# Kernel tuning notes

Measured on AMD Instinct MI355X. Metric: run time of the kernel, lower is better.

## Reference

```python
import jax, jax.numpy as jnp
import numpy as np

N_NODES = 500_000
N_EDGES = 16_000_000
F_IN, F_HID, F_OUT = 5, 5, 8


def _gcn_conv(x, W, b, src, dst, norm, n):
    # x: [N, Fin] -> transform first (cheaper than transforming messages)
    h = x @ W                              # [N, Fout]
    msg = h[src] * norm[:, None]           # [E', Fout] gather + per-edge scale
    out = jax.ops.segment_sum(msg, dst, num_segments=n)  # scatter-add over dst
    return out + b


def setup_inputs() -> dict:
    key = jax.random.key(0)
    ks = jax.random.split(key, 6)
    x = jax.random.normal(ks[0], (N_NODES, F_IN), dtype=jnp.float32)
    edge_index = jax.random.randint(ks[1], (2, N_EDGES), 0, N_NODES, dtype=jnp.int32)
    # Glorot-ish init for the two GCNConv layers
    W1 = jax.random.normal(ks[2], (F_IN, F_HID), dtype=jnp.float32) / np.sqrt(F_IN)
    b1 = jnp.zeros((F_HID,), dtype=jnp.float32)
    W2 = jax.random.normal(ks[3], (F_HID, F_OUT), dtype=jnp.float32) / np.sqrt(F_HID)
    b2 = jnp.zeros((F_OUT,), dtype=jnp.float32)
    return {"x": x, "edge_index": edge_index, "W1": W1, "b1": b1, "W2": W2, "b2": b2}


def reference(x, edge_index, W1, b1, W2, b2):
    n = x.shape[0]
    # GCNConv default: add self-loops, symmetric D^-1/2 A D^-1/2 normalization
    loops = jnp.arange(n, dtype=edge_index.dtype)
    src = jnp.concatenate([edge_index[0], loops])
    dst = jnp.concatenate([edge_index[1], loops])
    deg = jax.ops.segment_sum(jnp.ones_like(dst, dtype=x.dtype), dst, num_segments=n)
    dinv = jnp.where(deg > 0, jax.lax.rsqrt(deg), 0.0)
    norm = dinv[src] * dinv[dst]           # [E + N]

    h = _gcn_conv(x, W1, b1, src, dst, norm, n)
    h = jax.nn.relu(h)
    # F.dropout with training=False is the identity (eval-mode reference)
    h = _gcn_conv(h, W2, b2, src, dst, norm, n)
    return jax.nn.log_softmax(h, axis=1)
```

## Files before the change

### kernel.cpp

```cpp
#include <hip/hip_runtime.h>
#include <math.h>


#define FIN 5
#define FHID 5
#define FOUT 8
#define RB 256
#define EPA 24576
#define NBUCK_MAX 2048
#define OCAP 10240

typedef _Float16 half8 __attribute__((ext_vector_type(8)));
typedef int int4v __attribute__((ext_vector_type(4)));
typedef float fl4 __attribute__((ext_vector_type(4)));


__global__ void k_scan1(const int* __restrict__ t, int* __restrict__ scn,
                        int* __restrict__ partial, int n) {
    __shared__ int sh[256];
    int tx = threadIdx.x;
    int i = blockIdx.x * 256 + tx;
    int v = (i < n) ? t[i] : 0;
    sh[tx] = v;
    __syncthreads();
    for (int off = 1; off < 256; off <<= 1) {
        int add = (tx >= off) ? sh[tx - off] : 0;
        __syncthreads();
        sh[tx] += add;
        __syncthreads();
    }
    if (i < n) scn[i] = sh[tx] - v;
    if (tx == 255) partial[blockIdx.x] = sh[255];
}

__global__ void k_scan2(int* __restrict__ partial, int nb) {
    __shared__ int sh[256];
    __shared__ int carry;
    int tx = threadIdx.x;
    if (tx == 0) carry = 0;
    __syncthreads();
    for (int base = 0; base < nb; base += 256) {
        int i = base + tx;
        int v = (i < nb) ? partial[i] : 0;
        int c0 = carry;
        sh[tx] = v;
        __syncthreads();
        for (int off = 1; off < 256; off <<= 1) {
            int add = (tx >= off) ? sh[tx - off] : 0;
            __syncthreads();
            sh[tx] += add;
            __syncthreads();
        }
        if (i < nb) partial[i] = c0 + sh[tx] - v;
        __syncthreads();
        if (tx == 0) carry = c0 + sh[255];
        __syncthreads();
    }
}


__global__ void k_histA(const int* __restrict__ dst, int* __restrict__ cnt,
                        int e, int nbuck, int nblkA) {
    __shared__ int hist[NBUCK_MAX];
    int tx = threadIdx.x, blk = blockIdx.x;
    for (int b = tx; b < nbuck; b += 1024) hist[b] = 0;
    __syncthreads();
    size_t base = (size_t)blk * EPA;
    const int4v* dst4 = (const int4v*)dst;
    for (int k = 0; k < EPA / 4096; ++k) {
        size_t e4 = base / 4 + (size_t)k * 1024 + tx;
        size_t i = e4 * 4;
        if (i + 3 < (size_t)e) {
            int4v d4 = __builtin_nontemporal_load(&dst4[e4]);
#pragma unroll
            for (int j = 0; j < 4; ++j) atomicAdd(&hist[d4[j] >> 8], 1);
        } else {
            for (int j = 0; j < 4; ++j) {
                size_t ii = i + j;
                if (ii < (size_t)e) atomicAdd(&hist[dst[ii] >> 8], 1);
            }
        }
    }
    __syncthreads();
    for (int b = tx; b < nbuck; b += 1024) cnt[(size_t)b * nblkA + blk] = hist[b];
}

__global__ void k_scatterA(const int* __restrict__ src, const int* __restrict__ dst,
                           const int* __restrict__ cnt,
                           const int* __restrict__ scn, const int* __restrict__ part,
                           unsigned int* __restrict__ binnedA,
                           int e, int nbuck, int nblkA) {
    __shared__ int lstart[NBUCK_MAX];
    __shared__ int cur[NBUCK_MAX];
    __shared__ int gbase[NBUCK_MAX];
    __shared__ unsigned int staged[EPA];
    int tx = threadIdx.x, blk = blockIdx.x;
    for (int b = tx; b < NBUCK_MAX; b += 1024) {
        if (b < nbuck) {
            size_t idx = (size_t)b * nblkA + blk;
            lstart[b] = cnt[idx];
            gbase[b] = scn[idx] + part[idx >> 8];
        } else {
            lstart[b] = 0;
        }
    }
    __syncthreads();
    int j0 = tx, j1 = tx + 1024;
    int c0 = lstart[j0], c1 = lstart[j1];
    for (int off = 1; off < NBUCK_MAX; off <<= 1) {
        int a0 = (j0 >= off) ? lstart[j0 - off] : 0;
        int a1 = (j1 >= off) ? lstart[j1 - off] : 0;
        __syncthreads();
        lstart[j0] += a0; lstart[j1] += a1;
        __syncthreads();
    }
    int e0 = lstart[j0] - c0, e1 = lstart[j1] - c1;
    __syncthreads();
    lstart[j0] = e0; lstart[j1] = e1;
    cur[j0] = e0;    cur[j1] = e1;
    __syncthreads();
    size_t base = (size_t)blk * EPA;
    const int4v* dst4 = (const int4v*)dst;
    const int4v* src4 = (const int4v*)src;
    for (int k = 0; k < EPA / 4096; ++k) {
        size_t e4 = base / 4 + (size_t)k * 1024 + tx;
        size_t i = e4 * 4;
        if (i + 3 < (size_t)e) {
            int4v d4 = __builtin_nontemporal_load(&dst4[e4]);
            int4v s4 = __builtin_nontemporal_load(&src4[e4]);
#pragma unroll
            for (int j = 0; j < 4; ++j) {
                int d = d4[j];
                int pos = atomicAdd(&cur[d >> 8], 1);
                staged[pos] = ((unsigned int)(d & (RB - 1)) << 19) | (unsigned int)s4[j];
            }
        } else {
            for (int j = 0; j < 4; ++j) {
                size_t ii = i + j;
                if (ii < (size_t)e) {
                    int d = dst[ii];
                    int pos = atomicAdd(&cur[d >> 8], 1);
                    staged[pos] = ((unsigned int)(d & (RB - 1)) << 19) | (unsigned int)src[ii];
                }
            }
        }
    }
    __syncthreads();
    int grp = tx >> 4, lane = tx & 15;
    for (int b = grp; b < nbuck; b += 64) {
        int ls = lstart[b];
        int le = (b + 1 < NBUCK_MAX) ? lstart[b + 1] : 0;
        int len = le - ls;
        int gb = gbase[b];
        for (int k = lane; k < len; k += 16)
            binnedA[gb + k] = staged[ls + k];
    }
}


__global__ void k_passC(const unsigned int* __restrict__ binnedA,
                        const int* __restrict__ scn, const int* __restrict__ part,
                        const float* __restrict__ x,
                        half8* __restrict__ g1, unsigned int* __restrict__ binned3,
                        int* __restrict__ nodeptr, int* __restrict__ midptr,
                        int n, int e, int nbuck, int nblkA, unsigned int half) {
    __shared__ int hist[2 * RB];
    __shared__ int scanbuf[2 * RB];
    __shared__ int cur[2 * RB];
    __shared__ unsigned int obuf[OCAP];
    int tx = threadIdx.x, b = blockIdx.x;
    hist[tx] = 0;
    __syncthreads();
    size_t i0 = (size_t)b * nblkA;
    int start = scn[i0] + part[i0 >> 8];
    int end;
    if (b + 1 < nbuck) {
        size_t i1 = (size_t)(b + 1) * nblkA;
        end = scn[i1] + part[i1 >> 8];
    } else {
        end = e;
    }
    int len = end - start;
    for (int i = start + tx; i < end; i += 512) {
        unsigned int p = binnedA[i];
        int key = (int)((p >> 19) << 1) | ((p & 0x7FFFFu) >= half ? 1 : 0);
        atomicAdd(&hist[key], 1);
    }
    __syncthreads();
    int v = hist[tx];
    scanbuf[tx] = v;
    __syncthreads();
    for (int off = 1; off < 2 * RB; off <<= 1) {
        int add = (tx >= off) ? scanbuf[tx - off] : 0;
        __syncthreads();
        scanbuf[tx] += add;
        __syncthreads();
    }
    int excl = scanbuf[tx] - v;
    cur[tx] = excl;
    if ((tx & 1) == 0) nodeptr[(size_t)b * RB + (tx >> 1)] = start + excl;
    else               midptr[(size_t)b * RB + (tx >> 1)]  = start + excl;
    if (tx < RB) {
        int node = b * RB + tx;
        if (node < n) {
            int deg = hist[2 * tx] + hist[2 * tx + 1];
            float d = rsqrtf((float)(deg + 1));
            const float* xp = x + (size_t)node * FIN;
            half8 row = {};
#pragma unroll
            for (int f = 0; f < FIN; ++f) row[f] = (_Float16)(xp[f] * d);
            row[5] = (_Float16)d;
            g1[node] = row;
        }
    }
    if (b == nbuck - 1 && tx == 0) nodeptr[(size_t)nbuck * RB] = end;
    __syncthreads();
    if (len <= OCAP) {
        for (int i = start + tx; i < end; i += 512) {
            unsigned int p = binnedA[i];
            int key = (int)((p >> 19) << 1) | ((p & 0x7FFFFu) >= half ? 1 : 0);
            int pos = atomicAdd(&cur[key], 1);
            obuf[pos] = p & 0x7FFFFu;
        }
        __syncthreads();
        for (int j = tx; j < len; j += 512)
            binned3[start + j] = obuf[j];
    } else {
        for (int i = start + tx; i < end; i += 512) {
            unsigned int p = binnedA[i];
            int key = (int)((p >> 19) << 1) | ((p & 0x7FFFFu) >= half ? 1 : 0);
            int pos = atomicAdd(&cur[key], 1);
            binned3[start + pos] = p & 0x7FFFFu;
        }
    }
}


__global__ void k_vphase0(const unsigned int* __restrict__ ed,
                          const int* __restrict__ nodeptr, const int* __restrict__ midptr,
                          const half8* __restrict__ g,
                          fl4* __restrict__ acc4, float* __restrict__ acc1, int n) {
    int tid = blockIdx.x * blockDim.x + threadIdx.x;
    int node = tid >> 4;
    int lane = tid & 15;
    if (node >= n) return;
    int o0 = nodeptr[node];
    int om = midptr[node];
    float a0 = 0, a1 = 0, a2 = 0, a3 = 0, a4 = 0;
    for (int k = o0 + lane; k < om; k += 16) {
        unsigned int s = __builtin_nontemporal_load(&ed[k]);
        half8 hv = g[s];
        a0 += (float)hv[0]; a1 += (float)hv[1]; a2 += (float)hv[2];
        a3 += (float)hv[3]; a4 += (float)hv[4];
    }
#pragma unroll
    for (int off = 1; off < 16; off <<= 1) {
        a0 += __shfl_xor(a0, off, 16);
        a1 += __shfl_xor(a1, off, 16);
        a2 += __shfl_xor(a2, off, 16);
        a3 += __shfl_xor(a3, off, 16);
        a4 += __shfl_xor(a4, off, 16);
    }
    if (lane == 0) {
        fl4 p; p.x = a0; p.y = a1; p.z = a2; p.w = a3;
        __builtin_nontemporal_store(p, &acc4[node]);
        __builtin_nontemporal_store(a4, &acc1[node]);
    }
}

__global__ void k_vp1_l1(const unsigned int* __restrict__ ed,
                         const int* __restrict__ nodeptr, const int* __restrict__ midptr,
                         const half8* __restrict__ g1,
                         const fl4* __restrict__ acc4, const float* __restrict__ acc1,
                         const float* __restrict__ W1, const float* __restrict__ b1,
                         half8* __restrict__ g2, int n) {
    int tid = blockIdx.x * blockDim.x + threadIdx.x;
    int node = tid >> 4;
    int lane = tid & 15;
    if (node >= n) return;
    int om = midptr[node];
    int o1 = nodeptr[node + 1];
    float a0 = 0, a1 = 0, a2 = 0, a3 = 0, a4 = 0;
    for (int k = om + lane; k < o1; k += 16) {
        unsigned int s = __builtin_nontemporal_load(&ed[k]);
        half8 hv = g1[s];
        a0 += (float)hv[0]; a1 += (float)hv[1]; a2 += (float)hv[2];
        a3 += (float)hv[3]; a4 += (float)hv[4];
    }
#pragma unroll
    for (int off = 1; off < 16; off <<= 1) {
        a0 += __shfl_xor(a0, off, 16);
        a1 += __shfl_xor(a1, off, 16);
        a2 += __shfl_xor(a2, off, 16);
        a3 += __shfl_xor(a3, off, 16);
        a4 += __shfl_xor(a4, off, 16);
    }
    if (lane == 0) {
        fl4 pp = acc4[node];
        float p4 = acc1[node];
        half8 gi = g1[node];
        float d = (float)gi[5];
        float v[FIN];
        v[0] = (a0 + pp.x + (float)gi[0]) * d;
        v[1] = (a1 + pp.y + (float)gi[1]) * d;
        v[2] = (a2 + pp.z + (float)gi[2]) * d;
        v[3] = (a3 + pp.w + (float)gi[3]) * d;
        v[4] = (a4 + p4   + (float)gi[4]) * d;
        half8 go = {};
#pragma unroll
        for (int j = 0; j < FHID; ++j) {
            float s = b1[j];
#pragma unroll
            for (int k = 0; k < FIN; ++k) s = fmaf(v[k], W1[k * FHID + j], s);
            go[j] = (_Float16)(fmaxf(s, 0.0f) * d);
        }
        go[5] = gi[5];
        g2[node] = go;
    }
}

__global__ void k_vp1_l2(const unsigned int* __restrict__ ed,
                         const int* __restrict__ nodeptr, const int* __restrict__ midptr,
                         const half8* __restrict__ g2,
                         const fl4* __restrict__ acc4, const float* __restrict__ acc1,
                         const float* __restrict__ W2, const float* __restrict__ b2,
                         float* __restrict__ out, int n) {
    int tid = blockIdx.x * blockDim.x + threadIdx.x;
    int node = tid >> 4;
    int lane = tid & 15;
    if (node >= n) return;
    int om = midptr[node];
    int o1 = nodeptr[node + 1];
    float a0 = 0, a1 = 0, a2 = 0, a3 = 0, a4 = 0;
    for (int k = om + lane; k < o1; k += 16) {
        unsigned int s = __builtin_nontemporal_load(&ed[k]);
        half8 hv = g2[s];
        a0 += (float)hv[0]; a1 += (float)hv[1]; a2 += (float)hv[2];
        a3 += (float)hv[3]; a4 += (float)hv[4];
    }
#pragma unroll
    for (int off = 1; off < 16; off <<= 1) {
        a0 += __shfl_xor(a0, off, 16);
        a1 += __shfl_xor(a1, off, 16);
        a2 += __shfl_xor(a2, off, 16);
        a3 += __shfl_xor(a3, off, 16);
        a4 += __shfl_xor(a4, off, 16);
    }
    if (lane == 0) {
        fl4 pp = acc4[node];
        float p4 = acc1[node];
        half8 gi = g2[node];
        float d = (float)gi[5];
        float v[FHID];
        v[0] = (a0 + pp.x + (float)gi[0]) * d;
        v[1] = (a1 + pp.y + (float)gi[1]) * d;
        v[2] = (a2 + pp.z + (float)gi[2]) * d;
        v[3] = (a3 + pp.w + (float)gi[3]) * d;
        v[4] = (a4 + p4   + (float)gi[4]) * d;
        float o[FOUT];
        float m = -1e30f;
#pragma unroll
        for (int j = 0; j < FOUT; ++j) {
            float s = b2[j];
#pragma unroll
            for (int k = 0; k < FHID; ++k) s = fmaf(v[k], W2[k * FOUT + j], s);
            o[j] = s;
            m = fmaxf(m, s);
        }
        float ssum = 0.0f;
#pragma unroll
        for (int j = 0; j < FOUT; ++j) ssum += expf(o[j] - m);
        float lse = m + logf(ssum);
        float* op = out + (size_t)node * FOUT;
#pragma unroll
        for (int j = 0; j < FOUT; ++j) op[j] = o[j] - lse;
    }
}


__global__ void f_init_deg(float* __restrict__ deg, int n) {
    int i = blockIdx.x * blockDim.x + threadIdx.x;
    if (i < n) deg[i] = 1.0f;
}
__global__ void f_count_deg(const int* __restrict__ dst, float* __restrict__ deg, int e) {
    int i = blockIdx.x * blockDim.x + threadIdx.x;
    if (i < e) atomicAdd(&deg[dst[i]], 1.0f);
}
__global__ void f_finish_deg_g1(const float* __restrict__ x, float* __restrict__ dinv,
                                float* __restrict__ g1, int n) {
    int i = blockIdx.x * blockDim.x + threadIdx.x;
    if (i >= n) return;
    float d = rsqrtf(dinv[i]);
    dinv[i] = d;
#pragma unroll
    for (int f = 0; f < FIN; ++f) g1[(size_t)i * FIN + f] = x[(size_t)i * FIN + f] * d;
}
__global__ void f_scatter5(const int* __restrict__ src, const int* __restrict__ dst,
                           const float* __restrict__ g, float* __restrict__ acc, int e) {
    int i = blockIdx.x * blockDim.x + threadIdx.x;
    if (i >= e) return;
    int s = src[i], d = dst[i];
    float* a = acc + (size_t)d * 5;
    const float* gp = g + (size_t)s * 5;
    atomicAdd(a + 0, gp[0]);
    atomicAdd(a + 1, gp[1]);
    atomicAdd(a + 2, gp[2]);
    atomicAdd(a + 3, gp[3]);
    atomicAdd(a + 4, gp[4]);
}
__global__ void f_update1(const float* __restrict__ dinv, float* __restrict__ g,
                          float* __restrict__ acc, const float* __restrict__ W1,
                          const float* __restrict__ b1, int n) {
    int i = blockIdx.x * blockDim.x + threadIdx.x;
    if (i >= n) return;
    float d = dinv[i];
    float v[FIN];
#pragma unroll
    for (int f = 0; f < FIN; ++f) {
        size_t idx = (size_t)i * FIN + f;
        v[f] = (acc[idx] + g[idx]) * d;
        acc[idx] = 0.0f;
    }
#pragma unroll
    for (int j = 0; j < FHID; ++j) {
        float s = b1[j];
#pragma unroll
        for (int k = 0; k < FIN; ++k) s += v[k] * W1[k * FHID + j];
        g[(size_t)i * FHID + j] = fmaxf(s, 0.0f) * d;
    }
}
__global__ void f_update2(const float* __restrict__ dinv, const float* __restrict__ g,
                          const float* __restrict__ acc, const float* __restrict__ W2,
                          const float* __restrict__ b2, float* __restrict__ out, int n) {
    int i = blockIdx.x * blockDim.x + threadIdx.x;
    if (i >= n) return;
    float d = dinv[i];
    float v[FHID];
#pragma unroll
    for (int f = 0; f < FHID; ++f) v[f] = (acc[(size_t)i * FHID + f] + g[(size_t)i * FHID + f]) * d;
    float o[FOUT];
    float m = -1e30f;
#pragma unroll
    for (int j = 0; j < FOUT; ++j) {
        float s = b2[j];
#pragma unroll
        for (int k = 0; k < FHID; ++k) s += v[k] * W2[k * FOUT + j];
        o[j] = s;
        m = fmaxf(m, s);
    }
    float ssum = 0.0f;
#pragma unroll
    for (int j = 0; j < FOUT; ++j) ssum += expf(o[j] - m);
    float lse = m + logf(ssum);
#pragma unroll
    for (int j = 0; j < FOUT; ++j) out[(size_t)i * FOUT + j] = o[j] - lse;
}


extern "C" void kernel_launch(void* const* d_in, const int* in_sizes, int n_in,
                              void* d_out, int out_size, void* d_ws, size_t ws_size,
                              hipStream_t stream) {
    const float* x  = (const float*)d_in[0];
    const int*   ei = (const int*)d_in[1];
    const float* W1 = (const float*)d_in[2];
    const float* b1 = (const float*)d_in[3];
    const float* W2 = (const float*)d_in[4];
    const float* b2 = (const float*)d_in[5];

    const int n = in_sizes[0] / FIN;
    const int e = in_sizes[1] / 2;
    const int* src = ei;
    const int* dst = ei + e;

    const int nbuck = (n + RB - 1) / RB;
    const int nblkA = (e + EPA - 1) / EPA;
    const size_t m = (size_t)nbuck * nblkA;
    const int nsb = (int)((m + 255) / 256);

    size_t off = 0;
    auto al = [&](size_t bytes) { size_t o = off; off = (off + bytes + 15) & ~(size_t)15; return o; };
    int*          cnt     = (int*)((char*)d_ws + al(m * 4));
    int*          scn     = (int*)((char*)d_ws + al(m * 4));
    int*          part    = (int*)((char*)d_ws + al((size_t)nsb * 4));
    int*          nptr    = (int*)((char*)d_ws + al(((size_t)nbuck * RB + 1) * 4));
    int*          mptr    = (int*)((char*)d_ws + al((size_t)nbuck * RB * 4));
    half8*        g1      = (half8*)((char*)d_ws + al((size_t)n * 16));
    unsigned int* binnedA = (unsigned int*)((char*)d_ws + al((size_t)e * 4));
    unsigned int* binned3 = (unsigned int*)((char*)d_ws + al((size_t)e * 4));
    half8*        g2      = (half8*)binnedA;
    fl4*          acc4    = (fl4*)((char*)binnedA + (size_t)16 * 1024 * 1024);
    float*        acc1    = (float*)((char*)binnedA + (size_t)32 * 1024 * 1024);
    const size_t need = off;

    if (ws_size >= need && n <= 524288 && n >= 1 && (e & 3) == 0 && nbuck <= NBUCK_MAX &&
        (size_t)e * 4 >= (size_t)34 * 1024 * 1024 && (size_t)n * 16 <= (size_t)16 * 1024 * 1024) {
        const unsigned int half = (unsigned int)(n >> 1);
        k_histA<<<nblkA, 1024, 0, stream>>>(dst, cnt, e, nbuck, nblkA);
        k_scan1<<<nsb, 256, 0, stream>>>(cnt, scn, part, (int)m);
        k_scan2<<<1, 256, 0, stream>>>(part, nsb);
        k_scatterA<<<nblkA, 1024, 0, stream>>>(src, dst, cnt, scn, part, binnedA, e, nbuck, nblkA);
        k_passC<<<nbuck, 512, 0, stream>>>(binnedA, scn, part, x, g1, binned3, nptr, mptr,
                                           n, e, nbuck, nblkA, half);
        const int ga = (int)(((size_t)n * 16 + 511) / 512);
        k_vphase0<<<ga, 512, 0, stream>>>(binned3, nptr, mptr, g1, acc4, acc1, n);
        k_vp1_l1<<<ga, 512, 0, stream>>>(binned3, nptr, mptr, g1, acc4, acc1, W1, b1, g2, n);
        k_vphase0<<<ga, 512, 0, stream>>>(binned3, nptr, mptr, g2, acc4, acc1, n);
        k_vp1_l2<<<ga, 512, 0, stream>>>(binned3, nptr, mptr, g2, acc4, acc1, W2, b2, (float*)d_out, n);
        return;
    }

    const int B = 256;
    const int gn = (n + B - 1) / B;
    const int ge = (e + B - 1) / B;
    float* fdinv = (float*)d_ws;
    float* fg    = fdinv + n;
    float* facc  = fg + (size_t)5 * n;
    hipMemsetAsync(facc, 0, (size_t)5 * n * sizeof(float), stream);
    f_init_deg<<<gn, B, 0, stream>>>(fdinv, n);
    f_count_deg<<<ge, B, 0, stream>>>(dst, fdinv, e);
    f_finish_deg_g1<<<gn, B, 0, stream>>>(x, fdinv, fg, n);
    f_scatter5<<<ge, B, 0, stream>>>(src, dst, fg, facc, e);
    f_update1<<<gn, B, 0, stream>>>(fdinv, fg, facc, W1, b1, n);
    f_scatter5<<<ge, B, 0, stream>>>(src, dst, fg, facc, e);
    f_update2<<<gn, B, 0, stream>>>(fdinv, fg, facc, W2, b2, (float*)d_out, n);
}
```

Baseline: 489.8 us.

## Halve per-node lanes, scan counts in place, shrink scatter tile, parallelize softmax

The gather kernels now use 8 lanes per node instead of 16. The average degree is about 32, so this gives fewer idle lanes and half the thread count. The final layer spreads the 8 output logits and the log-softmax across the 8 lanes instead of running them serially in lane 0. The bucket-count scan now runs in place, and scatterA derives local counts from adjacent scanned offsets, which drops one workspace array and one read. EPA is halved, which doubles the number of scatter blocks and cuts shared staging per block; in exchange the count matrix and the scan work get larger.

```diff
diff --git a/kernel.cpp b/kernel.cpp
--- a/kernel.cpp
+++ b/kernel.cpp
@@ -6,7 +6,7 @@
 #define FHID 5
 #define FOUT 8
 #define RB 256
-#define EPA 24576
+#define EPA 12288
 #define NBUCK_MAX 2048
 #define OCAP 10240
 
@@ -15,12 +15,11 @@
 typedef float fl4 __attribute__((ext_vector_type(4)));
 
 
-__global__ void k_scan1(const int* __restrict__ t, int* __restrict__ scn,
-                        int* __restrict__ partial, int n) {
+__global__ void k_scan1(int* __restrict__ data, int* __restrict__ partial, int n) {
     __shared__ int sh[256];
     int tx = threadIdx.x;
     int i = blockIdx.x * 256 + tx;
-    int v = (i < n) ? t[i] : 0;
+    int v = (i < n) ? data[i] : 0;
     sh[tx] = v;
     __syncthreads();
     for (int off = 1; off < 256; off <<= 1) {
@@ -29,7 +28,7 @@
         sh[tx] += add;
         __syncthreads();
     }
-    if (i < n) scn[i] = sh[tx] - v;
+    if (i < n) data[i] = sh[tx] - v;
     if (tx == 255) partial[blockIdx.x] = sh[255];
 }
 
@@ -86,7 +85,6 @@
 }
 
 __global__ void k_scatterA(const int* __restrict__ src, const int* __restrict__ dst,
-                           const int* __restrict__ cnt,
                            const int* __restrict__ scn, const int* __restrict__ part,
                            unsigned int* __restrict__ binnedA,
                            int e, int nbuck, int nblkA) {
@@ -95,11 +93,15 @@
     __shared__ int gbase[NBUCK_MAX];
     __shared__ unsigned int staged[EPA];
     int tx = threadIdx.x, blk = blockIdx.x;
+    const size_t mm = (size_t)nbuck * nblkA;
     for (int b = tx; b < NBUCK_MAX; b += 1024) {
         if (b < nbuck) {
             size_t idx = (size_t)b * nblkA + blk;
-            lstart[b] = cnt[idx];
-            gbase[b] = scn[idx] + part[idx >> 8];
+            int s0 = scn[idx] + part[idx >> 8];
+            size_t idx1 = idx + 1;
+            int s1 = (idx1 < mm) ? (scn[idx1] + part[idx1 >> 8]) : e;
+            gbase[b] = s0;
+            lstart[b] = s1 - s0;
         } else {
             lstart[b] = 0;
         }
@@ -146,13 +148,13 @@
         }
     }
     __syncthreads();
-    int grp = tx >> 4, lane = tx & 15;
-    for (int b = grp; b < nbuck; b += 64) {
+    int grp = tx >> 3, lane = tx & 7;
+    for (int b = grp; b < nbuck; b += 128) {
         int ls = lstart[b];
         int le = (b + 1 < NBUCK_MAX) ? lstart[b + 1] : 0;
         int len = le - ls;
         int gb = gbase[b];
-        for (int k = lane; k < len; k += 16)
+        for (int k = lane; k < len; k += 8)
             binnedA[gb + k] = staged[ls + k];
     }
 }
@@ -241,25 +243,25 @@
                           const half8* __restrict__ g,
                           fl4* __restrict__ acc4, float* __restrict__ acc1, int n) {
     int tid = blockIdx.x * blockDim.x + threadIdx.x;
-    int node = tid >> 4;
-    int lane = tid & 15;
+    int node = tid >> 3;
+    int lane = tid & 7;
     if (node >= n) return;
     int o0 = nodeptr[node];
     int om = midptr[node];
     float a0 = 0, a1 = 0, a2 = 0, a3 = 0, a4 = 0;
-    for (int k = o0 + lane; k < om; k += 16) {
+    for (int k = o0 + lane; k < om; k += 8) {
         unsigned int s = __builtin_nontemporal_load(&ed[k]);
         half8 hv = g[s];
         a0 += (float)hv[0]; a1 += (float)hv[1]; a2 += (float)hv[2];
         a3 += (float)hv[3]; a4 += (float)hv[4];
     }
 #pragma unroll
-    for (int off = 1; off < 16; off <<= 1) {
-        a0 += __shfl_xor(a0, off, 16);
-        a1 += __shfl_xor(a1, off, 16);
-        a2 += __shfl_xor(a2, off, 16);
-        a3 += __shfl_xor(a3, off, 16);
-        a4 += __shfl_xor(a4, off, 16);
+    for (int off = 1; off < 8; off <<= 1) {
+        a0 += __shfl_xor(a0, off, 8);
+        a1 += __shfl_xor(a1, off, 8);
+        a2 += __shfl_xor(a2, off, 8);
+        a3 += __shfl_xor(a3, off, 8);
+        a4 += __shfl_xor(a4, off, 8);
     }
     if (lane == 0) {
         fl4 p; p.x = a0; p.y = a1; p.z = a2; p.w = a3;
@@ -275,25 +277,25 @@
                          const float* __restrict__ W1, const float* __restrict__ b1,
                          half8* __restrict__ g2, int n) {
     int tid = blockIdx.x * blockDim.x + threadIdx.x;
-    int node = tid >> 4;
-    int lane = tid & 15;
+    int node = tid >> 3;
+    int lane = tid & 7;
     if (node >= n) return;
     int om = midptr[node];
     int o1 = nodeptr[node + 1];
     float a0 = 0, a1 = 0, a2 = 0, a3 = 0, a4 = 0;
-    for (int k = om + lane; k < o1; k += 16) {
+    for (int k = om + lane; k < o1; k += 8) {
         unsigned int s = __builtin_nontemporal_load(&ed[k]);
         half8 hv = g1[s];
         a0 += (float)hv[0]; a1 += (float)hv[1]; a2 += (float)hv[2];
         a3 += (float)hv[3]; a4 += (float)hv[4];
     }
 #pragma unroll
-    for (int off = 1; off < 16; off <<= 1) {
-        a0 += __shfl_xor(a0, off, 16);
-        a1 += __shfl_xor(a1, off, 16);
-        a2 += __shfl_xor(a2, off, 16);
-        a3 += __shfl_xor(a3, off, 16);
-        a4 += __shfl_xor(a4, off, 16);
+    for (int off = 1; off < 8; off <<= 1) {
+        a0 += __shfl_xor(a0, off, 8);
+        a1 += __shfl_xor(a1, off, 8);
+        a2 += __shfl_xor(a2, off, 8);
+        a3 += __shfl_xor(a3, off, 8);
+        a4 += __shfl_xor(a4, off, 8);
     }
     if (lane == 0) {
         fl4 pp = acc4[node];
@@ -326,55 +328,47 @@
                          const float* __restrict__ W2, const float* __restrict__ b2,
                          float* __restrict__ out, int n) {
     int tid = blockIdx.x * blockDim.x + threadIdx.x;
-    int node = tid >> 4;
-    int lane = tid & 15;
+    int node = tid >> 3;
+    int lane = tid & 7;
     if (node >= n) return;
     int om = midptr[node];
     int o1 = nodeptr[node + 1];
     float a0 = 0, a1 = 0, a2 = 0, a3 = 0, a4 = 0;
-    for (int k = om + lane; k < o1; k += 16) {
+    for (int k = om + lane; k < o1; k += 8) {
         unsigned int s = __builtin_nontemporal_load(&ed[k]);
         half8 hv = g2[s];
         a0 += (float)hv[0]; a1 += (float)hv[1]; a2 += (float)hv[2];
         a3 += (float)hv[3]; a4 += (float)hv[4];
     }
 #pragma unroll
-    for (int off = 1; off < 16; off <<= 1) {
-        a0 += __shfl_xor(a0, off, 16);
-        a1 += __shfl_xor(a1, off, 16);
-        a2 += __shfl_xor(a2, off, 16);
-        a3 += __shfl_xor(a3, off, 16);
-        a4 += __shfl_xor(a4, off, 16);
-    }
-    if (lane == 0) {
-        fl4 pp = acc4[node];
-        float p4 = acc1[node];
-        half8 gi = g2[node];
-        float d = (float)gi[5];
-        float v[FHID];
-        v[0] = (a0 + pp.x + (float)gi[0]) * d;
-        v[1] = (a1 + pp.y + (float)gi[1]) * d;
-        v[2] = (a2 + pp.z + (float)gi[2]) * d;
-        v[3] = (a3 + pp.w + (float)gi[3]) * d;
-        v[4] = (a4 + p4   + (float)gi[4]) * d;
-        float o[FOUT];
-        float m = -1e30f;
-#pragma unroll
-        for (int j = 0; j < FOUT; ++j) {
-            float s = b2[j];
-#pragma unroll
-            for (int k = 0; k < FHID; ++k) s = fmaf(v[k], W2[k * FOUT + j], s);
-            o[j] = s;
-            m = fmaxf(m, s);
-        }
-        float ssum = 0.0f;
-#pragma unroll
-        for (int j = 0; j < FOUT; ++j) ssum += expf(o[j] - m);
-        float lse = m + logf(ssum);
-        float* op = out + (size_t)node * FOUT;
-#pragma unroll
-        for (int j = 0; j < FOUT; ++j) op[j] = o[j] - lse;
-    }
+    for (int off = 1; off < 8; off <<= 1) {
+        a0 += __shfl_xor(a0, off, 8);
+        a1 += __shfl_xor(a1, off, 8);
+        a2 += __shfl_xor(a2, off, 8);
+        a3 += __shfl_xor(a3, off, 8);
+        a4 += __shfl_xor(a4, off, 8);
+    }
+    fl4 pp = acc4[node];
+    float p4 = acc1[node];
+    half8 gi = g2[node];
+    float d = (float)gi[5];
+    float v[FHID];
+    v[0] = (a0 + pp.x + (float)gi[0]) * d;
+    v[1] = (a1 + pp.y + (float)gi[1]) * d;
+    v[2] = (a2 + pp.z + (float)gi[2]) * d;
+    v[3] = (a3 + pp.w + (float)gi[3]) * d;
+    v[4] = (a4 + p4   + (float)gi[4]) * d;
+    float oj = b2[lane];
+#pragma unroll
+    for (int k = 0; k < FHID; ++k) oj = fmaf(v[k], W2[k * FOUT + lane], oj);
+    float mx = oj;
+#pragma unroll
+    for (int off = 1; off < 8; off <<= 1) mx = fmaxf(mx, __shfl_xor(mx, off, 8));
+    float ex = expf(oj - mx);
+    float ss = ex;
+#pragma unroll
+    for (int off = 1; off < 8; off <<= 1) ss += __shfl_xor(ss, off, 8);
+    out[(size_t)node * FOUT + lane] = oj - mx - logf(ss);
 }
 
 
@@ -480,7 +474,6 @@
     size_t off = 0;
     auto al = [&](size_t bytes) { size_t o = off; off = (off + bytes + 15) & ~(size_t)15; return o; };
     int*          cnt     = (int*)((char*)d_ws + al(m * 4));
-    int*          scn     = (int*)((char*)d_ws + al(m * 4));
     int*          part    = (int*)((char*)d_ws + al((size_t)nsb * 4));
     int*          nptr    = (int*)((char*)d_ws + al(((size_t)nbuck * RB + 1) * 4));
     int*          mptr    = (int*)((char*)d_ws + al((size_t)nbuck * RB * 4));
@@ -496,12 +489,12 @@
         (size_t)e * 4 >= (size_t)34 * 1024 * 1024 && (size_t)n * 16 <= (size_t)16 * 1024 * 1024) {
         const unsigned int half = (unsigned int)(n >> 1);
         k_histA<<<nblkA, 1024, 0, stream>>>(dst, cnt, e, nbuck, nblkA);
-        k_scan1<<<nsb, 256, 0, stream>>>(cnt, scn, part, (int)m);
+        k_scan1<<<nsb, 256, 0, stream>>>(cnt, part, (int)m);
         k_scan2<<<1, 256, 0, stream>>>(part, nsb);
-        k_scatterA<<<nblkA, 1024, 0, stream>>>(src, dst, cnt, scn, part, binnedA, e, nbuck, nblkA);
-        k_passC<<<nbuck, 512, 0, stream>>>(binnedA, scn, part, x, g1, binned3, nptr, mptr,
+        k_scatterA<<<nblkA, 1024, 0, stream>>>(src, dst, cnt, part, binnedA, e, nbuck, nblkA);
+        k_passC<<<nbuck, 512, 0, stream>>>(binnedA, cnt, part, x, g1, binned3, nptr, mptr,
                                            n, e, nbuck, nblkA, half);
-        const int ga = (int)(((size_t)n * 16 + 511) / 512);
+        const int ga = (int)(((size_t)n * 8 + 511) / 512);
         k_vphase0<<<ga, 512, 0, stream>>>(binned3, nptr, mptr, g1, acc4, acc1, n);
         k_vp1_l1<<<ga, 512, 0, stream>>>(binned3, nptr, mptr, g1, acc4, acc1, W1, b1, g2, n);
         k_vphase0<<<ga, 512, 0, stream>>>(binned3, nptr, mptr, g2, acc4, acc1, n);
```

Result: slower. 522.4 us (+6.7%).
